# Optimization experiments

Hardware: AMD Instinct MI355X
Metric: run time of the kernel (lower is better)

Reference implementation:

```python
import jax, jax.numpy as jnp
import numpy as np

B, L, N, E = 512, 50, 64, 16
H = 128
D = 2 * H
ITEM_NUM, CATE_NUM = 100000, 500
STEP = 2
EPS = 1e-12


def l2norm(x):
    # F.normalize(p=2): x / max(||x||, eps)
    n = jnp.sqrt(jnp.sum(x * x, axis=-1, keepdims=True))
    return x / jnp.maximum(n, EPS)


def setup_inputs() -> dict:
    key = jax.random.key(0)
    ks = jax.random.split(key, 16)
    stdv = 1.0 / np.sqrt(H)
    u = lambda k, sh: jax.random.uniform(k, sh, jnp.float32, -stdv, stdv)
    embedding = u(ks[0], (ITEM_NUM + CATE_NUM, H)).at[0].set(0.0)  # padding_idx=0
    item_seq = jax.random.randint(ks[1], (B, L), 1, ITEM_NUM)
    label = jax.random.randint(ks[2], (B,), 1, ITEM_NUM)
    nodes = jax.random.randint(ks[3], (B, N), 1, ITEM_NUM + CATE_NUM)
    hn_adj = (jax.random.uniform(ks[4], (B, N, E)) < 0.25).astype(jnp.float32)
    alias_item = jax.random.randint(ks[5], (B, L), 0, N)
    alias_cate = jax.random.randint(ks[6], (B, L), 0, N)
    item_cates = jax.random.randint(ks[7], (ITEM_NUM,), ITEM_NUM, ITEM_NUM + CATE_NUM)
    return {
        'item_seq': item_seq, 'label': label, 'nodes': nodes, 'hn_adj': hn_adj,
        'alias_item': alias_item, 'alias_cate': alias_cate,
        'embedding': embedding, 'item_cates': item_cates,
        'w_edge': u(ks[8], (H, H)), 'w_node': u(ks[9], (H, H)),
        'q1_w': u(ks[10], (D, D)), 'q1_b': u(ks[11], (D,)),
        'q2_w': u(ks[12], (D, D)), 'v_w': u(ks[13], (D, 1)),
    }


def hgnn(n_h, adj, w_edge, w_node):
    # degree-normalized node->hyperedge->node propagation, STEP iterations
    deg_e = jnp.maximum(adj.sum(axis=1)[:, :, None], 1.0)  # [B,E,1]
    deg_n = jnp.maximum(adj.sum(axis=2)[:, :, None], 1.0)  # [B,N,1]
    e_h = None
    for _ in range(STEP):
        e_h = (jnp.einsum('bne,bnd->bed', adj, n_h) / deg_e) @ w_edge  # [B,E,H]
        n_h = (jnp.einsum('bne,bed->bnd', adj, e_h) / deg_n) @ w_node  # [B,N,H]
    return n_h, e_h


def nodes2items(nodes_hidden, alias):
    # batched gather: nodes_hidden[b, alias[b, l]] -> [B, L, H]
    return jnp.take_along_axis(nodes_hidden, alias[:, :, None], axis=1)


def last_attention(seq_hidden, mask, q1_w, q1_b, q2_w, v_w):
    # SR-GNN-style readout: query = hidden at last valid position
    last_idx = jnp.maximum(mask.sum(axis=1) - 1, 0)  # [B]
    ht = jnp.take_along_axis(seq_hidden, last_idx[:, None, None], axis=1)[:, 0]  # [B,D]
    q1 = ht @ q1_w                     # [B,D]
    q2 = seq_hidden @ q2_w             # [B,L,D]
    alpha = jax.nn.sigmoid(q1[:, None, :] + q2 + q1_b) @ v_w  # [B,L,1]
    m = mask[:, :, None].astype(seq_hidden.dtype)
    return jnp.sum(alpha * seq_hidden * m, axis=1)  # [B,D]


def reference(item_seq, label, nodes, hn_adj, alias_item, alias_cate,
              embedding, item_cates, w_edge, w_node, q1_w, q1_b, q2_w, v_w):
    mask = item_seq > 0  # [B,L]
    nodes_hidden_in = l2norm(embedding[nodes])  # [B,N,H] (dropout=identity, eval)
    nodes_hidden, _edges_hidden = hgnn(nodes_hidden_in, hn_adj, w_edge, w_node)
    item_seq_hidden = nodes2items(nodes_hidden, alias_item)  # [B,L,H]
    cate_seq_hidden = nodes2items(nodes_hidden, alias_cate)  # [B,L,H]
    seq_hidden = l2norm(jnp.concatenate([item_seq_hidden, cate_seq_hidden], axis=-1))
    seq_output = last_attention(seq_hidden, mask, q1_w, q1_b, q2_w, v_w)  # [B,2H]
    item_emb = jnp.concatenate([embedding[:ITEM_NUM], embedding[item_cates]], axis=-1)
    scores = l2norm(seq_output) @ l2norm(item_emb).T  # [B,item_num]
    return scores * 16.0
```

## Files before the change

kernel.cpp:

```cpp
#include <hip/hip_runtime.h>

typedef __bf16 bf16;
typedef float f32x4 __attribute__((ext_vector_type(4)));
typedef bf16 bf16x8 __attribute__((ext_vector_type(8)));

#define BB 512
#define LL 50
#define NN 64
#define EE 16
#define HH 128
#define DD 256
#define ITEMS 100000
#define EPSV 1e-12f

__global__ void k_detect(const unsigned int* __restrict__ adj_words, int* __restrict__ flag) {
    __shared__ int s;
    if (threadIdx.x == 0) s = 0;
    __syncthreads();
    int local = 0;
    for (int i = 0; i < 16; i++) {
        unsigned int w = adj_words[threadIdx.x * 16 + i];
        if (w != 0u && w != 0x3F800000u) local = 1;
    }
    if (local) s = 1;
    __syncthreads();
    if (threadIdx.x == 0) flag[0] = s;
}

template <typename T>
__device__ __forceinline__ void nodes_norm_body(const int* nodes, const T* emb, float* nodes_h) {
    int row  = blockIdx.x * 4 + (threadIdx.x >> 6);
    int lane = threadIdx.x & 63;
    int node = nodes[row];
    const T* src = emb + (long)node * HH;
    float x0 = (float)src[lane * 2], x1 = (float)src[lane * 2 + 1];
    float s = x0 * x0 + x1 * x1;
    for (int o = 32; o; o >>= 1) s += __shfl_xor(s, o);
    float inv = 1.0f / fmaxf(sqrtf(s), EPSV);
    float* dst = nodes_h + (long)row * HH;
    dst[lane * 2] = x0 * inv;
    dst[lane * 2 + 1] = x1 * inv;
}
__global__ void k_nodes_norm(const int* __restrict__ nodes, const void* __restrict__ emb,
                             const int* __restrict__ flag, float* __restrict__ nodes_h) {
    if (*flag) nodes_norm_body<bf16>(nodes, (const bf16*)emb, nodes_h);
    else       nodes_norm_body<float>(nodes, (const float*)emb, nodes_h);
}

template <typename T>
__device__ __forceinline__ void hgnn_body(const T* hn_adj, const T* w_edge, const T* w_node,
                                          float* nodes_h, float (*s_nh)[HH], float (*s_ea)[HH],
                                          float (*s_eh)[HH], float (*s_adj)[EE],
                                          float* s_rde, float* s_rdn) {
    int b = blockIdx.x, t = threadIdx.x;
    float* nh_g = nodes_h + (long)b * NN * HH;
    for (int i = t; i < NN * HH / 4; i += 256)
        ((f32x4*)s_nh)[i] = ((const f32x4*)nh_g)[i];
    const T* adj_g = hn_adj + (long)b * NN * EE;
    for (int i = t; i < NN * EE; i += 256)
        ((float*)s_adj)[i] = (float)adj_g[i];
    __syncthreads();
    if (t < EE) {
        float s = 0;
        for (int n = 0; n < NN; n++) s += s_adj[n][t];
        s_rde[t] = 1.0f / fmaxf(s, 1.0f);
    } else if (t >= 64 && t < 64 + NN) {
        int n = t - 64;
        float s = 0;
        for (int e = 0; e < EE; e++) s += s_adj[n][e];
        s_rdn[n] = 1.0f / fmaxf(s, 1.0f);
    }
    __syncthreads();
    int d = t & 127, half = t >> 7;
    for (int step = 0; step < 2; step++) {
        for (int i = 0; i < 8; i++) {
            int e = half * 8 + i;
            float acc = 0;
            for (int n = 0; n < NN; n++) acc += s_adj[n][e] * s_nh[n][d];
            s_ea[e][d] = acc * s_rde[e];
        }
        __syncthreads();
        {
            float acc[8] = {0, 0, 0, 0, 0, 0, 0, 0};
            for (int k = 0; k < HH; k++) {
                float wv = (float)w_edge[k * HH + d];
                for (int i = 0; i < 8; i++) acc[i] += s_ea[half * 8 + i][k] * wv;
            }
            for (int i = 0; i < 8; i++) s_eh[half * 8 + i][d] = acc[i];
        }
        __syncthreads();
        {
            float acc[8] = {0, 0, 0, 0, 0, 0, 0, 0};
            for (int k = 0; k < HH; k++) {
                float wv = (float)w_node[k * HH + d];
                for (int i = 0; i < 8; i++) acc[i] += s_eh[half * 8 + i][k] * wv;
            }
            for (int i = 0; i < 8; i++) s_ea[half * 8 + i][d] = acc[i];
        }
        __syncthreads();
        for (int i = 0; i < 32; i++) {
            int n = half * 32 + i;
            float acc = 0;
            for (int e = 0; e < EE; e++) acc += s_adj[n][e] * s_ea[e][d];
            s_nh[n][d] = acc * s_rdn[n];
        }
        __syncthreads();
    }
    for (int i = t; i < NN * HH / 4; i += 256)
        ((f32x4*)nh_g)[i] = ((f32x4*)s_nh)[i];
}
__global__ __launch_bounds__(256) void k_hgnn(const void* __restrict__ hn_adj,
                                              const void* __restrict__ w_edge,
                                              const void* __restrict__ w_node,
                                              const int* __restrict__ flag,
                                              float* __restrict__ nodes_h) {
    __shared__ float s_nh[NN][HH];
    __shared__ float s_ea[EE][HH];
    __shared__ float s_eh[EE][HH];
    __shared__ float s_adj[NN][EE];
    __shared__ float s_rde[EE], s_rdn[NN];
    if (*flag) hgnn_body<bf16>((const bf16*)hn_adj, (const bf16*)w_edge, (const bf16*)w_node,
                               nodes_h, s_nh, s_ea, s_eh, s_adj, s_rde, s_rdn);
    else       hgnn_body<float>((const float*)hn_adj, (const float*)w_edge, (const float*)w_node,
                                nodes_h, s_nh, s_ea, s_eh, s_adj, s_rde, s_rdn);
}

__global__ void k_seq_hidden(const int* __restrict__ alias_item, const int* __restrict__ alias_cate,
                             const float* __restrict__ nodes_h, float* __restrict__ seq_h) {
    int row  = blockIdx.x * 4 + (threadIdx.x >> 6);
    int lane = threadIdx.x & 63;
    int b = row / LL;
    int ai = alias_item[row], ac = alias_cate[row];
    const float* iv = nodes_h + ((long)b * NN + ai) * HH;
    const float* cv = nodes_h + ((long)b * NN + ac) * HH;
    float x0 = iv[lane * 2], x1 = iv[lane * 2 + 1];
    float y0 = cv[lane * 2], y1 = cv[lane * 2 + 1];
    float s = x0 * x0 + x1 * x1 + y0 * y0 + y1 * y1;
    for (int o = 32; o; o >>= 1) s += __shfl_xor(s, o);
    float inv = 1.0f / fmaxf(sqrtf(s), EPSV);
    float* dst = seq_h + (long)row * DD;
    dst[lane * 2] = x0 * inv;
    dst[lane * 2 + 1] = x1 * inv;
    dst[128 + lane * 2] = y0 * inv;
    dst[128 + lane * 2 + 1] = y1 * inv;
}

template <typename T>
__device__ __forceinline__ void attn_body(const int* item_seq, const float* seq_h,
                                          const T* q1_w, const T* q1_b, const T* q2_w, const T* v_w,
                                          bf16* so_n, float (*s_sh)[DD], float* s_alpha,
                                          float* s_flag, float (*s_red)[32], int* s_li) {
    int b = blockIdx.x, t = threadIdx.x;
    const float* sh_g = seq_h + (long)b * LL * DD;
    for (int i = t; i < LL * DD / 4; i += 256)
        ((f32x4*)s_sh)[i] = ((const f32x4*)sh_g)[i];
    if (t < LL) s_flag[t] = (item_seq[b * LL + t] > 0) ? 1.0f : 0.0f;
    __syncthreads();
    if (t == 0) {
        int c = 0;
        for (int l = 0; l < LL; l++) c += (s_flag[l] > 0.5f);
        *s_li = max(c - 1, 0);
    }
    __syncthreads();
    int li = *s_li;
    int d = t;
    float q1d = (float)q1_b[d];
    for (int k = 0; k < DD; k++) q1d += s_sh[li][k] * (float)q1_w[k * DD + d];
    float vwd = (float)v_w[d];
    int wv = t >> 6, lane = t & 63;
    for (int p = 0; p < 2; p++) {
        float acc[25];
        for (int i = 0; i < 25; i++) acc[i] = 0;
        int l0 = p * 25;
        for (int k = 0; k < DD; k++) {
            float wkd = (float)q2_w[k * DD + d];
            for (int i = 0; i < 25; i++) acc[i] += s_sh[l0 + i][k] * wkd;
        }
        for (int i = 0; i < 25; i++) {
            float val = 1.0f / (1.0f + __expf(-(q1d + acc[i])));
            float contrib = val * vwd;
            for (int o = 32; o; o >>= 1) contrib += __shfl_xor(contrib, o);
            if (lane == 0) s_red[wv][i] = contrib;
        }
        __syncthreads();
        if (t < 25) s_alpha[l0 + t] = s_red[0][t] + s_red[1][t] + s_red[2][t] + s_red[3][t];
        __syncthreads();
    }
    float so = 0;
    for (int l = 0; l < LL; l++) so += s_alpha[l] * s_flag[l] * s_sh[l][d];
    float ss = so * so;
    for (int o = 32; o; o >>= 1) ss += __shfl_xor(ss, o);
    if (lane == 0) s_red[0][wv] = ss;
    __syncthreads();
    float tot = s_red[0][0] + s_red[0][1] + s_red[0][2] + s_red[0][3];
    float inv = 1.0f / fmaxf(sqrtf(tot), EPSV);
    so_n[b * DD + d] = (bf16)(so * inv);
}
__global__ __launch_bounds__(256) void k_attn(const int* __restrict__ item_seq,
                                              const float* __restrict__ seq_h,
                                              const void* __restrict__ q1_w, const void* __restrict__ q1_b,
                                              const void* __restrict__ q2_w, const void* __restrict__ v_w,
                                              const int* __restrict__ flag, bf16* __restrict__ so_n) {
    __shared__ float s_sh[LL][DD];
    __shared__ float s_alpha[LL];
    __shared__ float s_flag[LL];
    __shared__ float s_red[4][32];
    __shared__ int s_li;
    if (*flag) attn_body<bf16>(item_seq, seq_h, (const bf16*)q1_w, (const bf16*)q1_b,
                               (const bf16*)q2_w, (const bf16*)v_w, so_n,
                               s_sh, s_alpha, s_flag, s_red, &s_li);
    else       attn_body<float>(item_seq, seq_h, (const float*)q1_w, (const float*)q1_b,
                                (const float*)q2_w, (const float*)v_w, so_n,
                                s_sh, s_alpha, s_flag, s_red, &s_li);
}

#define NT 32
#define PAD 8
template <typename T, typename TO>
__device__ __forceinline__ void scores_body(const bf16* so_n, const T* emb, const int* item_cates,
                                            TO* out, bf16 (*sB)[DD + PAD], bf16 (*sA)[DD + PAD]) {
    int t = threadIdx.x;
    long n0 = (long)blockIdx.x * NT;
    {
        int r = t >> 3, j = t & 7;
        long item = n0 + r;
        int cate = item_cates[item];
        const T* ip = emb + item * HH;
        const T* cp = emb + (long)cate * HH;
        float v[32];
        for (int k = 0; k < 16; k++) v[k]      = (float)ip[j * 16 + k];
        for (int k = 0; k < 16; k++) v[16 + k] = (float)cp[j * 16 + k];
        float s = 0;
        for (int k = 0; k < 32; k++) s += v[k] * v[k];
        s += __shfl_xor(s, 1); s += __shfl_xor(s, 2); s += __shfl_xor(s, 4);
        float inv = 1.0f / fmaxf(sqrtf(s), EPSV);
        for (int k = 0; k < 16; k++) sB[r][j * 16 + k]       = (bf16)(v[k] * inv);
        for (int k = 0; k < 16; k++) sB[r][128 + j * 16 + k] = (bf16)(v[16 + k] * inv);
    }
    int w = t >> 6, lane = t & 63, quad = lane >> 4, r16 = lane & 15;
    for (int m0 = 0; m0 < 8; m0++) {
        int mbase = m0 * 64;
        __syncthreads();
        {
            int c = t & 31, r = t >> 5;
            for (int rr = r; rr < 64; rr += 8)
                *(f32x4*)&sA[rr][c * 8] = *(const f32x4*)&so_n[(long)(mbase + rr) * DD + c * 8];
        }
        __syncthreads();
        f32x4 acc0 = {0, 0, 0, 0}, acc1 = {0, 0, 0, 0};
        for (int kc = 0; kc < 8; kc++) {
            bf16x8 a  = *(bf16x8*)&sA[w * 16 + r16][kc * 32 + quad * 8];
            bf16x8 b0 = *(bf16x8*)&sB[r16][kc * 32 + quad * 8];
            bf16x8 b1 = *(bf16x8*)&sB[16 + r16][kc * 32 + quad * 8];
            acc0 = __builtin_amdgcn_mfma_f32_16x16x32_bf16(a, b0, acc0, 0, 0, 0);
            acc1 = __builtin_amdgcn_mfma_f32_16x16x32_bf16(a, b1, acc1, 0, 0, 0);
        }
        int row_base = mbase + w * 16 + quad * 4;
        for (int r = 0; r < 4; r++) {
            out[(long)(row_base + r) * ITEMS + n0 + r16]      = (TO)(acc0[r] * 16.0f);
            out[(long)(row_base + r) * ITEMS + n0 + r16 + 16] = (TO)(acc1[r] * 16.0f);
        }
    }
}
__global__ __launch_bounds__(256) void k_scores(const bf16* __restrict__ so_n,
                                                const void* __restrict__ emb,
                                                const int* __restrict__ item_cates,
                                                const int* __restrict__ flag,
                                                void* __restrict__ out) {
    __shared__ bf16 sB[NT][DD + PAD];
    __shared__ bf16 sA[64][DD + PAD];
    if (*flag) scores_body<bf16, bf16>(so_n, (const bf16*)emb, item_cates, (bf16*)out, sB, sA);
    else       scores_body<float, float>(so_n, (const float*)emb, item_cates, (float*)out, sB, sA);
}

extern "C" void kernel_launch(void* const* d_in, const int* in_sizes, int n_in,
                              void* d_out, int out_size, void* d_ws, size_t ws_size,
                              hipStream_t stream) {
    const int* item_seq   = (const int*)d_in[0];
    const int* nodes      = (const int*)d_in[2];
    const void* hn_adj    = d_in[3];
    const int* alias_item = (const int*)d_in[4];
    const int* alias_cate = (const int*)d_in[5];
    const void* emb       = d_in[6];
    const int* item_cates = (const int*)d_in[7];
    const void* w_edge    = d_in[8];
    const void* w_node    = d_in[9];
    const void* q1_w      = d_in[10];
    const void* q1_b      = d_in[11];
    const void* q2_w      = d_in[12];
    const void* v_w       = d_in[13];

    char* ws = (char*)d_ws;
    int*   flag    = (int*)ws;
    float* nodes_h = (float*)(ws + 256);
    float* seq_h   = (float*)(ws + 256 + 16777216);
    bf16*  so_n    = (bf16*)(ws + 256 + 16777216 + 26214400);

    k_detect<<<1, 256, 0, stream>>>((const unsigned int*)hn_adj, flag);
    k_nodes_norm<<<8192, 256, 0, stream>>>(nodes, emb, flag, nodes_h);
    k_hgnn<<<512, 256, 0, stream>>>(hn_adj, w_edge, w_node, flag, nodes_h);
    k_seq_hidden<<<6400, 256, 0, stream>>>(alias_item, alias_cate, nodes_h, seq_h);
    k_attn<<<512, 256, 0, stream>>>(item_seq, seq_h, q1_w, q1_b, q2_w, v_w, flag, so_n);
    k_scores<<<3125, 256, 0, stream>>>(so_n, emb, item_cates, flag, d_out);
}
```

Measured before the change: 571.5 us.

## Fuse seq-hidden gather into attention, use MFMA for q2 projection, register-cache score operands

Removes the separate seq_hidden kernel and its 26MB intermediate. The attention kernel now gathers and normalizes rows itself into bf16 shared memory and runs the q2 projection with bf16 MFMA against a pre-transposed q2 weight made by a new prep kernel. The scores kernel keeps B fragments in registers and reads A straight from global memory, dropping the per-chunk shared staging and barriers. k_detect switches to a ballot-based reduction. Lowering the q2 path to bf16 adds rounding error, and the query row is recomputed in fp32 from nodes_h.

```diff
diff --git a/kernel.cpp b/kernel.cpp
--- a/kernel.cpp
+++ b/kernel.cpp
@@ -3,6 +3,7 @@
 typedef __bf16 bf16;
 typedef float f32x4 __attribute__((ext_vector_type(4)));
 typedef bf16 bf16x8 __attribute__((ext_vector_type(8)));
+typedef bf16 bf16x4 __attribute__((ext_vector_type(4)));
 
 #define BB 512
 #define LL 50
@@ -14,17 +15,17 @@
 #define EPSV 1e-12f
 
 __global__ void k_detect(const unsigned int* __restrict__ adj_words, int* __restrict__ flag) {
-    __shared__ int s;
-    if (threadIdx.x == 0) s = 0;
-    __syncthreads();
+    __shared__ int s_w[4];
+    int t = threadIdx.x;
     int local = 0;
     for (int i = 0; i < 16; i++) {
-        unsigned int w = adj_words[threadIdx.x * 16 + i];
+        unsigned int w = adj_words[t * 16 + i];
         if (w != 0u && w != 0x3F800000u) local = 1;
     }
-    if (local) s = 1;
-    __syncthreads();
-    if (threadIdx.x == 0) flag[0] = s;
+    unsigned long long m = __ballot(local);
+    if ((t & 63) == 0) s_w[t >> 6] = (m != 0ull) ? 1 : 0;
+    __syncthreads();
+    if (t == 0) flag[0] = (s_w[0] | s_w[1] | s_w[2] | s_w[3]);
 }
 
 template <typename T>
@@ -125,37 +126,58 @@
                                 nodes_h, s_nh, s_ea, s_eh, s_adj, s_rde, s_rdn);
 }
 
-__global__ void k_seq_hidden(const int* __restrict__ alias_item, const int* __restrict__ alias_cate,
-                             const float* __restrict__ nodes_h, float* __restrict__ seq_h) {
-    int row  = blockIdx.x * 4 + (threadIdx.x >> 6);
-    int lane = threadIdx.x & 63;
-    int b = row / LL;
-    int ai = alias_item[row], ac = alias_cate[row];
-    const float* iv = nodes_h + ((long)b * NN + ai) * HH;
-    const float* cv = nodes_h + ((long)b * NN + ac) * HH;
-    float x0 = iv[lane * 2], x1 = iv[lane * 2 + 1];
-    float y0 = cv[lane * 2], y1 = cv[lane * 2 + 1];
-    float s = x0 * x0 + x1 * x1 + y0 * y0 + y1 * y1;
-    for (int o = 32; o; o >>= 1) s += __shfl_xor(s, o);
-    float inv = 1.0f / fmaxf(sqrtf(s), EPSV);
-    float* dst = seq_h + (long)row * DD;
-    dst[lane * 2] = x0 * inv;
-    dst[lane * 2 + 1] = x1 * inv;
-    dst[128 + lane * 2] = y0 * inv;
-    dst[128 + lane * 2 + 1] = y1 * inv;
-}
-
 template <typename T>
-__device__ __forceinline__ void attn_body(const int* item_seq, const float* seq_h,
-                                          const T* q1_w, const T* q1_b, const T* q2_w, const T* v_w,
-                                          bf16* so_n, float (*s_sh)[DD], float* s_alpha,
-                                          float* s_flag, float (*s_red)[32], int* s_li) {
+__device__ __forceinline__ void prep_body(const T* q2w, bf16* q2wT) {
+    int n = blockIdx.x, k = threadIdx.x;
+    q2wT[n * DD + k] = (bf16)(float)q2w[k * DD + n];
+}
+__global__ void k_prep(const void* __restrict__ q2w, const int* __restrict__ flag,
+                       bf16* __restrict__ q2wT) {
+    if (*flag) prep_body<bf16>((const bf16*)q2w, q2wT);
+    else       prep_body<float>((const float*)q2w, q2wT);
+}
+
+#define APAD 8
+template <typename T>
+__device__ __forceinline__ void attn_body(const int* item_seq, const int* alias_item,
+                                          const int* alias_cate, const float* nodes_h,
+                                          const T* q1_w, const T* q1_b, const T* v_w,
+                                          const bf16* q2wT, bf16* so_n,
+                                          bf16 (*sA)[DD + APAD], float* s_q1, float* s_vw,
+                                          float* s_ht, float (*s_alpha_w)[64], float* s_alpha,
+                                          float* s_flag, float* s_red, int* s_ai, int* s_ac,
+                                          int* s_li) {
     int b = blockIdx.x, t = threadIdx.x;
-    const float* sh_g = seq_h + (long)b * LL * DD;
-    for (int i = t; i < LL * DD / 4; i += 256)
-        ((f32x4*)s_sh)[i] = ((const f32x4*)sh_g)[i];
-    if (t < LL) s_flag[t] = (item_seq[b * LL + t] > 0) ? 1.0f : 0.0f;
-    __syncthreads();
+    int w = t >> 6, lane = t & 63, quad = lane >> 4, r16 = lane & 15;
+
+    if (t < LL) {
+        s_ai[t] = alias_item[b * LL + t];
+        s_ac[t] = alias_cate[b * LL + t];
+        s_flag[t] = (item_seq[b * LL + t] > 0) ? 1.0f : 0.0f;
+    }
+    s_vw[t] = (float)v_w[t];
+    __syncthreads();
+
+    for (int l = w; l < 64; l += 4) {
+        if (l < LL) {
+            const float* iv = nodes_h + ((long)b * NN + s_ai[l]) * HH;
+            const float* cv = nodes_h + ((long)b * NN + s_ac[l]) * HH;
+            float x0 = iv[lane * 2], x1 = iv[lane * 2 + 1];
+            float y0 = cv[lane * 2], y1 = cv[lane * 2 + 1];
+            float s = x0 * x0 + x1 * x1 + y0 * y0 + y1 * y1;
+            for (int o = 32; o; o >>= 1) s += __shfl_xor(s, o);
+            float inv = 1.0f / fmaxf(sqrtf(s), EPSV);
+            sA[l][lane * 2]       = (bf16)(x0 * inv);
+            sA[l][lane * 2 + 1]   = (bf16)(x1 * inv);
+            sA[l][128 + lane * 2]     = (bf16)(y0 * inv);
+            sA[l][128 + lane * 2 + 1] = (bf16)(y1 * inv);
+        } else {
+            sA[l][lane * 2]       = (bf16)0.f;
+            sA[l][lane * 2 + 1]   = (bf16)0.f;
+            sA[l][128 + lane * 2]     = (bf16)0.f;
+            sA[l][128 + lane * 2 + 1] = (bf16)0.f;
+        }
+    }
     if (t == 0) {
         int c = 0;
         for (int l = 0; l < LL; l++) c += (s_flag[l] > 0.5f);
@@ -163,62 +185,128 @@
     }
     __syncthreads();
     int li = *s_li;
-    int d = t;
-    float q1d = (float)q1_b[d];
-    for (int k = 0; k < DD; k++) q1d += s_sh[li][k] * (float)q1_w[k * DD + d];
-    float vwd = (float)v_w[d];
-    int wv = t >> 6, lane = t & 63;
-    for (int p = 0; p < 2; p++) {
-        float acc[25];
-        for (int i = 0; i < 25; i++) acc[i] = 0;
-        int l0 = p * 25;
-        for (int k = 0; k < DD; k++) {
-            float wkd = (float)q2_w[k * DD + d];
-            for (int i = 0; i < 25; i++) acc[i] += s_sh[l0 + i][k] * wkd;
-        }
-        for (int i = 0; i < 25; i++) {
-            float val = 1.0f / (1.0f + __expf(-(q1d + acc[i])));
-            float contrib = val * vwd;
-            for (int o = 32; o; o >>= 1) contrib += __shfl_xor(contrib, o);
-            if (lane == 0) s_red[wv][i] = contrib;
-        }
-        __syncthreads();
-        if (t < 25) s_alpha[l0 + t] = s_red[0][t] + s_red[1][t] + s_red[2][t] + s_red[3][t];
-        __syncthreads();
-    }
+
+    float htv;
+    {
+        int ai = s_ai[li], ac = s_ac[li];
+        htv = (t < 128) ? nodes_h[((long)b * NN + ai) * HH + t]
+                        : nodes_h[((long)b * NN + ac) * HH + (t - 128)];
+        float ss = htv * htv;
+        for (int o = 32; o; o >>= 1) ss += __shfl_xor(ss, o);
+        if (lane == 0) s_red[w] = ss;
+    }
+    __syncthreads();
+    {
+        float tot = s_red[0] + s_red[1] + s_red[2] + s_red[3];
+        s_ht[t] = htv / fmaxf(sqrtf(tot), EPSV);
+    }
+    __syncthreads();
+    {
+        float q1d = (float)q1_b[t];
+        for (int k = 0; k < DD; k++) q1d += s_ht[k] * (float)q1_w[k * DD + t];
+        s_q1[t] = q1d;
+    }
+    __syncthreads();
+
+    f32x4 acc[4][4];
+#pragma unroll
+    for (int mt = 0; mt < 4; mt++)
+#pragma unroll
+        for (int nt = 0; nt < 4; nt++) acc[mt][nt] = (f32x4){0, 0, 0, 0};
+#pragma unroll
+    for (int kc = 0; kc < 8; kc++) {
+        bf16x8 bfr[4], afr[4];
+#pragma unroll
+        for (int nt = 0; nt < 4; nt++)
+            bfr[nt] = *(const bf16x8*)&q2wT[(long)(w * 64 + nt * 16 + r16) * DD + kc * 32 + quad * 8];
+#pragma unroll
+        for (int mt = 0; mt < 4; mt++)
+            afr[mt] = *(const bf16x8*)&sA[mt * 16 + r16][kc * 32 + quad * 8];
+#pragma unroll
+        for (int mt = 0; mt < 4; mt++)
+#pragma unroll
+            for (int nt = 0; nt < 4; nt++)
+                acc[mt][nt] = __builtin_amdgcn_mfma_f32_16x16x32_bf16(afr[mt], bfr[nt], acc[mt][nt], 0, 0, 0);
+    }
+    float part[4][4];
+#pragma unroll
+    for (int mt = 0; mt < 4; mt++)
+#pragma unroll
+        for (int r = 0; r < 4; r++) part[mt][r] = 0.f;
+#pragma unroll
+    for (int nt = 0; nt < 4; nt++) {
+        int d = w * 64 + nt * 16 + r16;
+        float q1v = s_q1[d], vw = s_vw[d];
+#pragma unroll
+        for (int mt = 0; mt < 4; mt++)
+#pragma unroll
+            for (int r = 0; r < 4; r++) {
+                float sig = 1.0f / (1.0f + __expf(-(q1v + acc[mt][nt][r])));
+                part[mt][r] += sig * vw;
+            }
+    }
+#pragma unroll
+    for (int mt = 0; mt < 4; mt++)
+#pragma unroll
+        for (int r = 0; r < 4; r++) {
+            float v = part[mt][r];
+            v += __shfl_xor(v, 1); v += __shfl_xor(v, 2);
+            v += __shfl_xor(v, 4); v += __shfl_xor(v, 8);
+            part[mt][r] = v;
+        }
+    if (r16 == 0) {
+#pragma unroll
+        for (int mt = 0; mt < 4; mt++)
+#pragma unroll
+            for (int r = 0; r < 4; r++)
+                s_alpha_w[w][mt * 16 + quad * 4 + r] = part[mt][r];
+    }
+    __syncthreads();
+    if (t < 64) {
+        float a = s_alpha_w[0][t] + s_alpha_w[1][t] + s_alpha_w[2][t] + s_alpha_w[3][t];
+        s_alpha[t] = (t < LL) ? a * s_flag[t] : 0.f;
+    }
+    __syncthreads();
     float so = 0;
-    for (int l = 0; l < LL; l++) so += s_alpha[l] * s_flag[l] * s_sh[l][d];
+    for (int l = 0; l < LL; l++) so += s_alpha[l] * (float)sA[l][t];
     float ss = so * so;
     for (int o = 32; o; o >>= 1) ss += __shfl_xor(ss, o);
-    if (lane == 0) s_red[0][wv] = ss;
-    __syncthreads();
-    float tot = s_red[0][0] + s_red[0][1] + s_red[0][2] + s_red[0][3];
+    if (lane == 0) s_red[w] = ss;
+    __syncthreads();
+    float tot = s_red[0] + s_red[1] + s_red[2] + s_red[3];
     float inv = 1.0f / fmaxf(sqrtf(tot), EPSV);
-    so_n[b * DD + d] = (bf16)(so * inv);
+    so_n[b * DD + t] = (bf16)(so * inv);
 }
 __global__ __launch_bounds__(256) void k_attn(const int* __restrict__ item_seq,
-                                              const float* __restrict__ seq_h,
+                                              const int* __restrict__ alias_item,
+                                              const int* __restrict__ alias_cate,
+                                              const float* __restrict__ nodes_h,
                                               const void* __restrict__ q1_w, const void* __restrict__ q1_b,
-                                              const void* __restrict__ q2_w, const void* __restrict__ v_w,
+                                              const void* __restrict__ v_w, const bf16* __restrict__ q2wT,
                                               const int* __restrict__ flag, bf16* __restrict__ so_n) {
-    __shared__ float s_sh[LL][DD];
-    __shared__ float s_alpha[LL];
-    __shared__ float s_flag[LL];
-    __shared__ float s_red[4][32];
+    __shared__ bf16 sA[64][DD + APAD];
+    __shared__ float s_q1[DD], s_vw[DD], s_ht[DD];
+    __shared__ float s_alpha_w[4][64];
+    __shared__ float s_alpha[64];
+    __shared__ float s_flag[64];
+    __shared__ float s_red[4];
+    __shared__ int s_ai[64], s_ac[64];
     __shared__ int s_li;
-    if (*flag) attn_body<bf16>(item_seq, seq_h, (const bf16*)q1_w, (const bf16*)q1_b,
-                               (const bf16*)q2_w, (const bf16*)v_w, so_n,
-                               s_sh, s_alpha, s_flag, s_red, &s_li);
-    else       attn_body<float>(item_seq, seq_h, (const float*)q1_w, (const float*)q1_b,
-                                (const float*)q2_w, (const float*)v_w, so_n,
-                                s_sh, s_alpha, s_flag, s_red, &s_li);
+    if (*flag) attn_body<bf16>(item_seq, alias_item, alias_cate, nodes_h,
+                               (const bf16*)q1_w, (const bf16*)q1_b, (const bf16*)v_w,
+                               q2wT, so_n, sA, s_q1, s_vw, s_ht, s_alpha_w, s_alpha,
+                               s_flag, s_red, s_ai, s_ac, &s_li);
+    else       attn_body<float>(item_seq, alias_item, alias_cate, nodes_h,
+                                (const float*)q1_w, (const float*)q1_b, (const float*)v_w,
+                                q2wT, so_n, sA, s_q1, s_vw, s_ht, s_alpha_w, s_alpha,
+                                s_flag, s_red, s_ai, s_ac, &s_li);
 }
 
 #define NT 32
 #define PAD 8
 template <typename T, typename TO>
 __device__ __forceinline__ void scores_body(const bf16* so_n, const T* emb, const int* item_cates,
-                                            TO* out, bf16 (*sB)[DD + PAD], bf16 (*sA)[DD + PAD]) {
+                                            TO* out, bf16 (*sB)[DD + PAD]) {
     int t = threadIdx.x;
     long n0 = (long)blockIdx.x * NT;
     {
@@ -228,34 +316,42 @@
         const T* ip = emb + item * HH;
         const T* cp = emb + (long)cate * HH;
         float v[32];
+#pragma unroll
         for (int k = 0; k < 16; k++) v[k]      = (float)ip[j * 16 + k];
+#pragma unroll
         for (int k = 0; k < 16; k++) v[16 + k] = (float)cp[j * 16 + k];
         float s = 0;
+#pragma unroll
         for (int k = 0; k < 32; k++) s += v[k] * v[k];
         s += __shfl_xor(s, 1); s += __shfl_xor(s, 2); s += __shfl_xor(s, 4);
         float inv = 1.0f / fmaxf(sqrtf(s), EPSV);
+#pragma unroll
         for (int k = 0; k < 16; k++) sB[r][j * 16 + k]       = (bf16)(v[k] * inv);
+#pragma unroll
         for (int k = 0; k < 16; k++) sB[r][128 + j * 16 + k] = (bf16)(v[16 + k] * inv);
     }
+    __syncthreads();
     int w = t >> 6, lane = t & 63, quad = lane >> 4, r16 = lane & 15;
+    bf16x8 bf[2][8];
+#pragma unroll
+    for (int h = 0; h < 2; h++)
+#pragma unroll
+        for (int kc = 0; kc < 8; kc++)
+            bf[h][kc] = *(const bf16x8*)&sB[h * 16 + r16][kc * 32 + quad * 8];
     for (int m0 = 0; m0 < 8; m0++) {
-        int mbase = m0 * 64;
-        __syncthreads();
-        {
-            int c = t & 31, r = t >> 5;
-            for (int rr = r; rr < 64; rr += 8)
-                *(f32x4*)&sA[rr][c * 8] = *(const f32x4*)&so_n[(long)(mbase + rr) * DD + c * 8];
-        }
-        __syncthreads();
+        int mrow = m0 * 64 + w * 16 + r16;
+        const bf16* ap = so_n + (long)mrow * DD + quad * 8;
+        bf16x8 a[8];
+#pragma unroll
+        for (int kc = 0; kc < 8; kc++) a[kc] = *(const bf16x8*)(ap + kc * 32);
         f32x4 acc0 = {0, 0, 0, 0}, acc1 = {0, 0, 0, 0};
+#pragma unroll
         for (int kc = 0; kc < 8; kc++) {
-            bf16x8 a  = *(bf16x8*)&sA[w * 16 + r16][kc * 32 + quad * 8];
-            bf16x8 b0 = *(bf16x8*)&sB[r16][kc * 32 + quad * 8];
-            bf16x8 b1 = *(bf16x8*)&sB[16 + r16][kc * 32 + quad * 8];
-            acc0 = __builtin_amdgcn_mfma_f32_16x16x32_bf16(a, b0, acc0, 0, 0, 0);
-            acc1 = __builtin_amdgcn_mfma_f32_16x16x32_bf16(a, b1, acc1, 0, 0, 0);
-        }
-        int row_base = mbase + w * 16 + quad * 4;
+            acc0 = __builtin_amdgcn_mfma_f32_16x16x32_bf16(a[kc], bf[0][kc], acc0, 0, 0, 0);
+            acc1 = __builtin_amdgcn_mfma_f32_16x16x32_bf16(a[kc], bf[1][kc], acc1, 0, 0, 0);
+        }
+        int row_base = m0 * 64 + w * 16 + quad * 4;
+#pragma unroll
         for (int r = 0; r < 4; r++) {
             out[(long)(row_base + r) * ITEMS + n0 + r16]      = (TO)(acc0[r] * 16.0f);
             out[(long)(row_base + r) * ITEMS + n0 + r16 + 16] = (TO)(acc1[r] * 16.0f);
@@ -268,9 +364,8 @@
                                                 const int* __restrict__ flag,
                                                 void* __restrict__ out) {
     __shared__ bf16 sB[NT][DD + PAD];
-    __shared__ bf16 sA[64][DD + PAD];
-    if (*flag) scores_body<bf16, bf16>(so_n, (const bf16*)emb, item_cates, (bf16*)out, sB, sA);
-    else       scores_body<float, float>(so_n, (const float*)emb, item_cates, (float*)out, sB, sA);
+    if (*flag) scores_body<bf16, bf16>(so_n, (const bf16*)emb, item_cates, (bf16*)out, sB);
+    else       scores_body<float, float>(so_n, (const float*)emb, item_cates, (float*)out, sB);
 }
 
 extern "C" void kernel_launch(void* const* d_in, const int* in_sizes, int n_in,
@@ -292,14 +387,15 @@
 
     char* ws = (char*)d_ws;
     int*   flag    = (int*)ws;
-    float* nodes_h = (float*)(ws + 256);
-    float* seq_h   = (float*)(ws + 256 + 16777216);
-    bf16*  so_n    = (bf16*)(ws + 256 + 16777216 + 26214400);
+    bf16*  q2wT    = (bf16*)(ws + 256);
+    bf16*  so_n    = (bf16*)(ws + 131328);
+    float* nodes_h = (float*)(ws + 393472);
 
     k_detect<<<1, 256, 0, stream>>>((const unsigned int*)hn_adj, flag);
+    k_prep<<<256, 256, 0, stream>>>(q2_w, flag, q2wT);
     k_nodes_norm<<<8192, 256, 0, stream>>>(nodes, emb, flag, nodes_h);
     k_hgnn<<<512, 256, 0, stream>>>(hn_adj, w_edge, w_node, flag, nodes_h);
-    k_seq_hidden<<<6400, 256, 0, stream>>>(alias_item, alias_cate, nodes_h, seq_h);
-    k_attn<<<512, 256, 0, stream>>>(item_seq, seq_h, q1_w, q1_b, q2_w, v_w, flag, so_n);
+    k_attn<<<512, 256, 0, stream>>>(item_seq, alias_item, alias_cate, nodes_h,
+                                    q1_w, q1_b, v_w, q2wT, flag, so_n);
     k_scores<<<3125, 256, 0, stream>>>(so_n, emb, item_cates, flag, d_out);
 }
```

Measured after the change: 483.7 us. 15.4% less time.
